# Optimization experiments

Measured on AMD Instinct MI355X. Metric: run time of the kernel, lower is better.

The kernel has to match this reference:

```python
import jax, jax.numpy as jnp
import numpy as np

B, T, N = 16, 1024, 128
WIN, STEP = 30, 2
MOMENT_ORDERS = (2, 4, 8)
D_MODEL = 256


def _mask_diag(corr):
    n = corr.shape[-1]
    eye = jnp.eye(n, dtype=corr.dtype)
    return corr * (1.0 - eye) + eye


def corrcoef_time(xw):
    # xw: [..., L, N] -> corr over channels: [..., N, N]
    L = xw.shape[-2]
    xm = xw - xw.mean(axis=-2, keepdims=True)
    cov = jnp.einsum('...ln,...lm->...nm', xm, xm) / (L - 1 + 1e-8)
    var = jnp.clip(jnp.diagonal(cov, axis1=-2, axis2=-1), 1e-8, None)
    std = jnp.sqrt(var)
    corr = cov / (std[..., :, None] * std[..., None, :])
    corr = jnp.nan_to_num(corr, nan=0.0, posinf=0.0, neginf=0.0)
    return _mask_diag(corr)


def rowwise_corr(M):
    # M: [B, N, F]
    Xc = M - M.mean(axis=-1, keepdims=True)
    num = jnp.einsum('bnf,bmf->bnm', Xc, Xc)
    den1 = jnp.sqrt(jnp.clip((Xc ** 2).sum(axis=-1), 1e-8, None))
    corr = num / (den1[:, :, None] * den1[:, None, :])
    corr = jnp.nan_to_num(corr, nan=0.0, posinf=0.0, neginf=0.0)
    return _mask_diag(corr)


def layer_norm(x, gamma, beta, eps=1e-5):
    mu = x.mean(axis=-1, keepdims=True)
    var = ((x - mu) ** 2).mean(axis=-1, keepdims=True)
    return (x - mu) / jnp.sqrt(var + eps) * gamma + beta


def normalize_adj(adj):
    n = adj.shape[-1]
    A_hat = adj + jnp.eye(n, dtype=adj.dtype)
    d = A_hat.sum(axis=-1)
    dis = jnp.sqrt(1.0 / jnp.clip(d, 1e-8, None))
    return A_hat * dis[:, :, None] * dis[:, None, :]


def setup_inputs() -> dict:
    key = jax.random.key(0)
    ks = jax.random.split(key, 8)
    in_dim = len(MOMENT_ORDERS) * N
    return {
        'x': jax.random.normal(ks[0], (B, T, N), dtype=jnp.float32),
        'ln_gamma': jnp.ones((in_dim,), jnp.float32),
        'ln_beta': jnp.zeros((in_dim,), jnp.float32),
        'W1': jax.random.normal(ks[1], (in_dim, D_MODEL), jnp.float32) * 0.05,
        'b1': jnp.zeros((D_MODEL,), jnp.float32),
        'W2': jax.random.normal(ks[2], (D_MODEL, D_MODEL), jnp.float32) * 0.05,
        'b2': jnp.zeros((D_MODEL,), jnp.float32),
        'Wc': jax.random.normal(ks[3], (D_MODEL, 1), jnp.float32) * 0.05,
        'bc': jnp.zeros((1,), jnp.float32),
    }


def reference(x, ln_gamma, ln_beta, W1, b1, W2, b2, Wc, bc):
    # sliding windows (static indices)
    starts = np.arange(0, T - WIN + 1, STEP)
    idx = starts[:, None] + np.arange(WIN)[None, :]
    xw = x[:, idx, :]
    lo = corrcoef_time(xw)                            # [B, Wn, N, N]

    mean_lo = lo.mean(axis=1, keepdims=True)
    centered = lo - mean_lo
    cm_list, ho_list = [], []
    for d in MOMENT_ORDERS:
        cm = jnp.nan_to_num((centered ** d).mean(axis=1),
                            nan=0.0, posinf=0.0, neginf=0.0)  # [B, N, N]
        cm_list.append(cm)
        ho_list.append(rowwise_corr(cm))

    X = jnp.concatenate(cm_list, axis=-1)             # [B, N, 3N]
    X = layer_norm(X, ln_gamma, ln_beta)

    A = jnp.stack(ho_list, axis=1).mean(axis=1)
    A = 0.5 * (A + jnp.swapaxes(A, 1, 2))
    A_norm = normalize_adj(A)

    H = jax.nn.relu(jnp.einsum('bnm,bmd->bnd', A_norm, X @ W1 + b1))
    H = jax.nn.relu(jnp.einsum('bnm,bmd->bnd', A_norm, H @ W2 + b2))
    g = H.mean(axis=1)                                # [B, d_model]
    out = jax.nn.sigmoid(g @ Wc + bc)                 # [B, 1]
    return out
```

## Files before the change

### kernel.cpp

```cpp
#include <hip/hip_runtime.h>
#include <math.h>

#define BB  16
#define TT  1024
#define NN  128
#define WIN 30
#define NWD 498
#define DM  256
#define IND 384
#define GW  8

#define INV_W (1.0f/498.0f)

#define SARR (BB*NN*NN)

#define OFF_A     0
#define OFF_G     (OFF_A    + BB*NWD*NN)
#define OFF_CM2   (OFF_G    + BB*NWD*NN)
#define OFF_CM4   (OFF_CM2  + SARR)
#define OFF_CM8   (OFF_CM4  + SARR)
#define OFF_AD    (OFF_CM8  + SARR)
#define OFF_PART  (OFF_AD   + 3*SARR)
#define OFF_ANORM OFF_PART
#define OFF_BUFA  (OFF_ANORM + SARR)
#define OFF_BUFB  (OFF_BUFA + BB*NN*DM)
#define OFF_CTR   (OFF_PART + 768*16384)
#define OFF_GW1   OFF_A
#define OFF_SG    (OFF_GW1 + IND*DM)
#define OFF_SB    (OFF_SG  + DM)

#define GLL16(gsrc, ldst) \
    __builtin_amdgcn_global_load_lds((const __attribute__((address_space(1))) void*)(gsrc), \
                                     (__attribute__((address_space(3))) void*)(ldst), 16, 0, 0)

__global__ __launch_bounds__(128) void k1_stats(const float* __restrict__ x, float* __restrict__ ws) {
    int bx = blockIdx.x;
    if (bx == 0 && threadIdx.x < 128) ((unsigned*)(ws + OFF_CTR))[threadIdx.x] = 0u;
    int c = bx & 15, b = bx >> 4;
    int w0 = c*32, w1 = min(NWD, w0+32);
    int n = threadIdx.x;
    const float* xp = x + (size_t)b*TT*NN + n;

    float sum = 0.f, sq = 0.f;
    for (int t = 2*w0; t < 2*w0 + WIN; ++t) {
        float v = xp[(size_t)t*NN];
        sum += v; sq = fmaf(v, v, sq);
    }
    for (int w = w0; w < w1; ++w) {
        if (w > w0) {
            float o0 = xp[(size_t)(2*w-2)*NN], o1 = xp[(size_t)(2*w-1)*NN];
            float n0 = xp[(size_t)(2*w+28)*NN], n1 = xp[(size_t)(2*w+29)*NN];
            sum += (n0 + n1) - (o0 + o1);
            sq  += (n0*n0 + n1*n1) - (o0*o0 + o1*o1);
        }
        float mean = sum * (1.0f/30.0f);
        float ss = sq - 30.0f*mean*mean;
        float var = fmaxf(ss * (1.0f/29.0f), 1e-8f);
        float a = (1.0f / sqrtf(var)) * 0.185695338f;
        ws[OFF_A + ((size_t)b*NWD + w)*NN + n] = a;
        ws[OFF_G + ((size_t)b*NWD + w)*NN + n] = mean * a * 5.477225575f;
    }
}

__global__ __launch_bounds__(256) __attribute__((amdgpu_waves_per_eu(4, 4)))
void k24_inc(const float* __restrict__ x, float* __restrict__ ws) {
    __shared__ __align__(16) float xr[64][NN];
    __shared__ __align__(16) float sa[GW][NN];
    __shared__ __align__(16) float sg[GW][NN];
    int bx = blockIdx.x;
    int wc = bx & 7;
    int slab = (bx >> 3) % 6;
    int b = bx / 48;
    const char IS[6] = {0,0,0,0,1,1};
    const char JS[6] = {0,1,2,3,2,3};
    int is = IS[slab], js = JS[slab];
    int w0 = wc * 63, w1 = min(NWD, w0 + 63);
    int tid = threadIdx.x;
    int jg = tid & 7, ig = tid >> 3;
    int i0 = is*64 + ig*2;
    int j0 = js*32 + jg*4;

    const float* xb = x + (size_t)b*TT*NN;
    const float* Ab = ws + OFF_A + (size_t)b*NWD*NN;
    const float* Gb = ws + OFF_G + (size_t)b*NWD*NN;

    float P[2][4];
    float S1[2][4], S2[2][4], S3[2][4], S4[2][4], S5[2][4], S6[2][4], S7[2][4], S8[2][4];
#pragma unroll
    for (int p=0;p<2;++p)
#pragma unroll
        for (int q=0;q<4;++q) {
            P[p][q]=0.f;
            S1[p][q]=0.f;S2[p][q]=0.f;S3[p][q]=0.f;S4[p][q]=0.f;
            S5[p][q]=0.f;S6[p][q]=0.f;S7[p][q]=0.f;S8[p][q]=0.f;
        }

    auto moments = [&](int k) {
        float2 ai = *(const float2*)&sa[k][i0];
        float2 gi = *(const float2*)&sg[k][i0];
        float4 aj = *(const float4*)&sa[k][j0];
        float4 gj = *(const float4*)&sg[k][j0];
        float av[2] = {ai.x, ai.y};
        float mg[2] = {-gi.x, -gi.y};
        float aw[4] = {aj.x, aj.y, aj.z, aj.w};
        float gw[4] = {gj.x, gj.y, gj.z, gj.w};
#pragma unroll
        for (int p=0;p<2;++p)
#pragma unroll
            for (int q=0;q<4;++q) {
                float aa  = av[p]*aw[q];
                float ngg = mg[p]*gw[q];
                float c   = fmaf(P[p][q], aa, ngg);
                float c2 = c*c;
                float c3 = c2*c;
                float c4 = c2*c2;
                S1[p][q] += c;
                S2[p][q] += c2;
                S3[p][q] += c3;
                S4[p][q] += c4;
                S5[p][q] = fmaf(c4, c,  S5[p][q]);
                S6[p][q] = fmaf(c3, c3, S6[p][q]);
                S7[p][q] = fmaf(c3, c4, S7[p][q]);
                S8[p][q] = fmaf(c4, c4, S8[p][q]);
            }
    };

    int rlo = 2*w0;
    for (int wg = w0; wg < w1; wg += GW) {
        int m = min(GW, w1 - wg);
        __syncthreads();
        int rhi = 2*(wg + m - 1) + 29;
        int nr = rhi - rlo + 1;
        for (int idx = tid; idx < nr*32; idx += 256) {
            int r = idx >> 5, c4 = idx & 31;
            int t = rlo + r;
            GLL16(xb + (size_t)t*NN + c4*4, &xr[t & 63][c4*4]);
        }
        for (int idx = tid; idx < m*32; idx += 256) {
            int k = idx >> 5, c4 = idx & 31;
            GLL16(Ab + (size_t)(wg+k)*NN + c4*4, &sa[k][c4*4]);
        }
        for (int idx = tid; idx < m*32; idx += 256) {
            int k = idx >> 5, c4 = idx & 31;
            GLL16(Gb + (size_t)(wg+k)*NN + c4*4, &sg[k][c4*4]);
        }
        rlo = rhi + 1;
        __syncthreads();

        int kstart = 0;
        if (wg == w0) {
#pragma unroll 6
            for (int k = 0; k < WIN; ++k) {
                int t = 2*w0 + k;
                float2 xi = *(const float2*)&xr[t & 63][i0];
                float4 xj = *(const float4*)&xr[t & 63][j0];
                float av[2] = {xi.x, xi.y};
                float bv[4] = {xj.x, xj.y, xj.z, xj.w};
#pragma unroll
                for (int p=0;p<2;++p)
#pragma unroll
                    for (int q=0;q<4;++q) P[p][q] = fmaf(av[p], bv[q], P[p][q]);
            }
            moments(0);
            kstart = 1;
        }
        for (int k = kstart; k < m; ++k) {
            int w = wg + k;
            int tr[4] = {2*w - 2, 2*w - 1, 2*w + 28, 2*w + 29};
#pragma unroll
            for (int kk = 0; kk < 4; ++kk) {
                int t = tr[kk];
                float sgn = (kk < 2) ? -1.0f : 1.0f;
                float2 xi = *(const float2*)&xr[t & 63][i0];
                float4 xj = *(const float4*)&xr[t & 63][j0];
                float av[2] = {sgn*xi.x, sgn*xi.y};
                float bv[4] = {xj.x, xj.y, xj.z, xj.w};
#pragma unroll
                for (int p=0;p<2;++p)
#pragma unroll
                    for (int q=0;q<4;++q) P[p][q] = fmaf(av[p], bv[q], P[p][q]);
            }
            moments(k);
        }
    }

    float* tp = ws + OFF_PART + (size_t)bx*16384 + tid*8;
#define STORE_ARR(A, S) \
    *(float4*)&tp[(A)*2048]     = make_float4(S[0][0], S[0][1], S[0][2], S[0][3]); \
    *(float4*)&tp[(A)*2048 + 4] = make_float4(S[1][0], S[1][1], S[1][2], S[1][3]);
    STORE_ARR(0, S1) STORE_ARR(1, S2) STORE_ARR(2, S3) STORE_ARR(3, S4)
    STORE_ARR(4, S5) STORE_ARR(5, S6) STORE_ARR(6, S7) STORE_ARR(7, S8)
#undef STORE_ARR
}

__global__ __launch_bounds__(256) void kred(const float* __restrict__ gamma, const float* __restrict__ beta,
                                            const float* __restrict__ W1, float* __restrict__ ws) {
    int bxg = blockIdx.x;
    int tid = threadIdx.x;
    if (bxg >= 192) {
        int gi = bxg - 192;
        if (gi < 96) {
#pragma unroll
            for (int kk = 0; kk < 4; ++kk) {
                int k = gi*4 + kk;
                ws[OFF_GW1 + (size_t)k*DM + tid] = gamma[k] * W1[(size_t)k*DM + tid];
            }
        } else {
            float sgv = 0.f, sbv = 0.f;
            for (int k = 0; k < IND; ++k) {
                float w = W1[(size_t)k*DM + tid];
                sgv = fmaf(gamma[k], w, sgv);
                sbv = fmaf(beta[k],  w, sbv);
            }
            ws[OFF_SG + tid] = sgv;
            ws[OFF_SB + tid] = sbv;
        }
        return;
    }
    int pair = bxg >> 1, half = bxg & 1;
    int b = pair / 6, slab = pair % 6;
    const char IS[6] = {0,0,0,0,1,1};
    const char JS[6] = {0,1,2,3,2,3};
    int is = IS[slab], js = JS[slab];
    int off4 = half*256 + tid;
    const float4* base = (const float4*)(ws + OFF_PART + (size_t)(b*48 + slab*8)*16384);

    float4 E[8];
#pragma unroll
    for (int a=0;a<8;++a) E[a] = make_float4(0.f,0.f,0.f,0.f);
    for (int c = 0; c < 8; ++c) {
        const float4* tp = base + (size_t)c*4096;
#pragma unroll
        for (int a=0;a<8;++a) {
            float4 v = tp[a*512 + off4];
            E[a].x += v.x; E[a].y += v.y; E[a].z += v.z; E[a].w += v.w;
        }
    }
    float Es[8][4];
#pragma unroll
    for (int a=0;a<8;++a) { Es[a][0]=E[a].x; Es[a][1]=E[a].y; Es[a][2]=E[a].z; Es[a][3]=E[a].w; }

    int tid_old = off4 >> 1, p = off4 & 1;
    int ig = tid_old >> 3, jg = tid_old & 7;
    int i  = is*64 + ig*2 + p;
    int j0 = js*32 + jg*4;
    float* C2 = ws + OFF_CM2 + (size_t)b*NN*NN;
    float* C4 = ws + OFF_CM4 + (size_t)b*NN*NN;
    float* C8 = ws + OFF_CM8 + (size_t)b*NN*NN;
#pragma unroll
    for (int l = 0; l < 4; ++l) {
        int j = j0 + l;
        float cm2, cm4, cm8;
        if (i == j) {
            cm2 = 0.f; cm4 = 0.f; cm8 = 0.f;
        } else {
            float e1 = Es[0][l]*INV_W, e2 = Es[1][l]*INV_W, e3 = Es[2][l]*INV_W, e4 = Es[3][l]*INV_W;
            float e5 = Es[4][l]*INV_W, e6 = Es[5][l]*INV_W, e7 = Es[6][l]*INV_W, e8 = Es[7][l]*INV_W;
            float m  = e1;
            float m2 = m*m, m3 = m2*m, m4 = m2*m2, m5 = m4*m, m6 = m3*m3, m8 = m4*m4;
            cm2 = e2 - m2;
            cm4 = e4 - 4.f*m*e3 + 6.f*m2*e2 - 3.f*m4;
            cm8 = e8 - 8.f*m*e7 + 28.f*m2*e6 - 56.f*m3*e5 + 70.f*m4*e4
                     - 56.f*m5*e3 + 28.f*m6*e2 - 7.f*m8;
        }
        C2[i*NN + j] = cm2; C2[j*NN + i] = cm2;
        C4[i*NN + j] = cm4; C4[j*NN + i] = cm4;
        C8[i*NN + j] = cm8; C8[j*NN + i] = cm8;
    }
}

#define XSTR 132
__global__ __launch_bounds__(256) void kB(const float* __restrict__ b1, float* __restrict__ ws) {
    __shared__ __align__(16) float smem[64*XSTR + 2*NN];
    __shared__ unsigned winB;
    int blk = blockIdx.x, tid = threadIdx.x;
    if (blk < 192) {
        int rem = blk % 12;
        int b = blk / 12, di = rem >> 2, jq = rem & 3;
        float* Xct = smem;
        float* Mr  = smem + 64*XSTR;
        float* Ir  = Mr + NN;
        const float* cm = ws + (di==0 ? OFF_CM2 : (di==1 ? OFF_CM4 : OFF_CM8)) + (size_t)b*NN*NN;
        int n0 = (tid >> 4)*8, m0 = jq*32 + (tid & 15)*2;
        float s1 = 0.f, s2 = 0.f;
        float acc0[8], acc1[8];
#pragma unroll
        for (int k=0;k<8;++k) { acc0[k]=0.f; acc1[k]=0.f; }

        for (int h = 0; h < 2; ++h) {
            __syncthreads();
            for (int idx = tid; idx < NN*64; idx += 256) {
                int n = idx >> 6, f0 = idx & 63;
                Xct[f0*XSTR + n] = cm[n*NN + h*64 + f0];
            }
            __syncthreads();
            if (tid < NN) {
                for (int f0 = 0; f0 < 64; ++f0) {
                    float v = Xct[f0*XSTR + tid];
                    s1 += v; s2 = fmaf(v, v, s2);
                }
            }
            for (int f0 = 0; f0 < 64; ++f0) {
                const float* row = &Xct[f0*XSTR];
                float4 a0 = *(const float4*)&row[n0];
                float4 a1 = *(const float4*)&row[n0+4];
                float2 bm = *(const float2*)&row[m0];
                float av[8] = {a0.x,a0.y,a0.z,a0.w,a1.x,a1.y,a1.z,a1.w};
#pragma unroll
                for (int k=0;k<8;++k) {
                    acc0[k] = fmaf(av[k], bm.x, acc0[k]);
                    acc1[k] = fmaf(av[k], bm.y, acc1[k]);
                }
            }
        }
        __syncthreads();
        if (tid < NN) {
            float mean = s1 * (1.0f/NN);
            Mr[tid] = mean;
            Ir[tid] = 1.0f/sqrtf(fmaxf(s2 - (float)NN*mean*mean, 1e-8f));
        }
        __syncthreads();
        float rm0 = Mr[m0], rm1 = Mr[m0+1], im0 = Ir[m0], im1 = Ir[m0+1];
        float* Ad = ws + OFF_AD + (size_t)(b*3 + di)*NN*NN;
#pragma unroll
        for (int k=0;k<8;++k) {
            int gi = n0+k;
            float rn = Mr[gi], inv = Ir[gi];
            float v0 = (acc0[k] - (float)NN*rn*rm0) * inv * im0;
            float v1 = (acc1[k] - (float)NN*rn*rm1) * inv * im1;
            if (gi == m0)   v0 = 1.0f;
            if (gi == m0+1) v1 = 1.0f;
            Ad[gi*NN + m0]     = v0;
            Ad[gi*NN + m0 + 1] = v1;
        }

        __syncthreads();
        if (tid == 0) {
            unsigned* ctr = (unsigned*)(ws + OFF_CTR);
            unsigned old = __hip_atomic_fetch_add(&ctr[96 + b], 1u,
                                                  __ATOMIC_ACQ_REL, __HIP_MEMORY_SCOPE_AGENT);
            winB = (old == 11u) ? 1u : 0u;
        }
        __syncthreads();
        if (winB) {
            float* dis = smem;
            const float* A0 = ws + OFF_AD + (size_t)(b*3 + 0)*NN*NN;
            const float* A1 = ws + OFF_AD + (size_t)(b*3 + 1)*NN*NN;
            const float* A2 = ws + OFF_AD + (size_t)(b*3 + 2)*NN*NN;
            if (tid < NN) {
                float d = 1.0f;
                for (int m = 0; m < NN; ++m) {
                    int o = tid*NN + m;
                    d += (A0[o] + A1[o] + A2[o]) * (1.0f/3.0f);
                }
                dis[tid] = sqrtf(1.0f / fmaxf(d, 1e-8f));
            }
            __syncthreads();
            float* An = ws + OFF_ANORM + (size_t)b*NN*NN;
            for (int idx = tid; idx < NN*NN; idx += 256) {
                int n = idx >> 7, m = idx & 127;
                float s = (A0[idx] + A1[idx] + A2[idx]) * (1.0f/3.0f);
                float v = s + (n==m ? 1.0f : 0.0f);
                An[idx] = v * dis[n] * dis[m];
            }
        }
    } else {
        int r0 = (blk - 192) * 4;
        float* sms = smem;
        float* srs = smem + 4;
        {
            int rloc = tid >> 6, lane = tid & 63;
            int grow = r0 + rloc;
            int b = grow >> 7, n = grow & 127;
            const float* c2 = ws + OFF_CM2 + ((size_t)b*NN + n)*NN;
            const float* c4 = ws + OFF_CM4 + ((size_t)b*NN + n)*NN;
            const float* c8 = ws + OFF_CM8 + ((size_t)b*NN + n)*NN;
            float s1 = 0.f, s2 = 0.f;
            for (int e = lane; e < IND; e += 64) {
                float v = (e < 128) ? c2[e] : (e < 256) ? c4[e-128] : c8[e-256];
                s1 += v; s2 = fmaf(v, v, s2);
            }
#pragma unroll
            for (int o = 32; o > 0; o >>= 1) {
                s1 += __shfl_down(s1, o, 64);
                s2 += __shfl_down(s2, o, 64);
            }
            if (lane == 0) {
                float mean = s1 * (1.0f/IND);
                sms[rloc] = mean;
                srs[rloc] = 1.0f / sqrtf(s2*(1.0f/IND) - mean*mean + 1e-5f);
            }
        }
        __syncthreads();
        float mean[4], rstd[4];
        const float* xrow[4];
#pragma unroll
        for (int r = 0; r < 4; ++r) {
            mean[r] = sms[r]; rstd[r] = srs[r];
        }
        float acc[4] = {0.f, 0.f, 0.f, 0.f};
        const float* GW1p = ws + OFF_GW1;
#pragma unroll
        for (int seg = 0; seg < 3; ++seg) {
            int offc = (seg==0) ? OFF_CM2 : (seg==1) ? OFF_CM4 : OFF_CM8;
#pragma unroll
            for (int r = 0; r < 4; ++r) {
                int grow = r0 + r;
                xrow[r] = ws + offc + ((size_t)(grow >> 7)*NN + (grow & 127))*NN;
            }
            const float* gseg = GW1p + (size_t)(seg*128)*DM + tid;
            for (int k = 0; k < 128; k += 2) {
                float g0 = gseg[(size_t)(k+0)*DM];
                float g1 = gseg[(size_t)(k+1)*DM];
#pragma unroll
                for (int r = 0; r < 4; ++r) {
                    acc[r] = fmaf(xrow[r][k+0], g0, acc[r]);
                    acc[r] = fmaf(xrow[r][k+1], g1, acc[r]);
                }
            }
        }
        float sgv = ws[OFF_SG + tid];
        float sbb = ws[OFF_SB + tid] + b1[tid];
        float* O = ws + OFF_BUFA;
#pragma unroll
        for (int r = 0; r < 4; ++r)
            O[(size_t)(r0+r)*DM + tid] = rstd[r]*(acc[r] - mean[r]*sgv) + sbb;
    }
}

__global__ __launch_bounds__(256) void k98_propgemm(const float* __restrict__ W2, const float* __restrict__ b2,
                                                    const float* __restrict__ An, const float* __restrict__ Zin,
                                                    float* __restrict__ Out) {
    __shared__ float Hs[4][DM];
    int bx = blockIdx.x;
    int b = bx >> 5, n0 = (bx & 31)*4;
    int tid = threadIdx.x;
    const float* A = An + (size_t)b*NN*NN + (size_t)n0*NN;
    const float* Z = Zin + (size_t)b*NN*DM;
    float acc[4] = {0,0,0,0};
    for (int m = 0; m < NN; m += 4) {
        float z0 = Z[(size_t)(m+0)*DM + tid];
        float z1 = Z[(size_t)(m+1)*DM + tid];
        float z2 = Z[(size_t)(m+2)*DM + tid];
        float z3 = Z[(size_t)(m+3)*DM + tid];
#pragma unroll
        for (int r = 0; r < 4; ++r) {
            const float* Ar = A + r*NN + m;
            acc[r] = fmaf(Ar[0], z0, acc[r]);
            acc[r] = fmaf(Ar[1], z1, acc[r]);
            acc[r] = fmaf(Ar[2], z2, acc[r]);
            acc[r] = fmaf(Ar[3], z3, acc[r]);
        }
    }
#pragma unroll
    for (int r = 0; r < 4; ++r) Hs[r][tid] = fmaxf(acc[r], 0.0f);
    __syncthreads();
    float acc2[4];
    float bv = b2[tid];
#pragma unroll
    for (int r = 0; r < 4; ++r) acc2[r] = bv;
    for (int k = 0; k < DM; k += 4) {
        float w0 = W2[(size_t)(k+0)*DM + tid];
        float w1 = W2[(size_t)(k+1)*DM + tid];
        float w2 = W2[(size_t)(k+2)*DM + tid];
        float w3 = W2[(size_t)(k+3)*DM + tid];
#pragma unroll
        for (int r = 0; r < 4; ++r) {
            float4 h = *(const float4*)&Hs[r][k];
            acc2[r] = fmaf(h.x, w0, acc2[r]);
            acc2[r] = fmaf(h.y, w1, acc2[r]);
            acc2[r] = fmaf(h.z, w2, acc2[r]);
            acc2[r] = fmaf(h.w, w3, acc2[r]);
        }
    }
    float* O = Out + (size_t)b*NN*DM;
#pragma unroll
    for (int r = 0; r < 4; ++r) O[(size_t)(n0+r)*DM + tid] = acc2[r];
}

__global__ __launch_bounds__(256) void k9_prop(const float* __restrict__ Wc, const float* __restrict__ bc,
                                               const float* __restrict__ An, const float* __restrict__ Zin,
                                               float* __restrict__ Out,
                                               float* __restrict__ ws, float* __restrict__ outp) {
    __shared__ float red[256];
    __shared__ unsigned win9;
    int bx = blockIdx.x;
    int b = bx >> 5, n0 = (bx & 31)*4;
    int tid = threadIdx.x;
    const float* A = An + (size_t)b*NN*NN + (size_t)n0*NN;
    const float* Z = Zin + (size_t)b*NN*DM;
    float acc[4] = {0,0,0,0};
    for (int m = 0; m < NN; m += 4) {
        float z0 = Z[(size_t)(m+0)*DM + tid];
        float z1 = Z[(size_t)(m+1)*DM + tid];
        float z2 = Z[(size_t)(m+2)*DM + tid];
        float z3 = Z[(size_t)(m+3)*DM + tid];
#pragma unroll
        for (int r = 0; r < 4; ++r) {
            const float* Ar = A + r*NN + m;
            acc[r] = fmaf(Ar[0], z0, acc[r]);
            acc[r] = fmaf(Ar[1], z1, acc[r]);
            acc[r] = fmaf(Ar[2], z2, acc[r]);
            acc[r] = fmaf(Ar[3], z3, acc[r]);
        }
    }
    float* O = Out + (size_t)b*NN*DM;
#pragma unroll
    for (int r = 0; r < 4; ++r) O[(size_t)(n0+r)*DM + tid] = fmaxf(acc[r], 0.0f);

    __syncthreads();
    if (tid == 0) {
        unsigned* ctr = (unsigned*)(ws + OFF_CTR);
        unsigned old = __hip_atomic_fetch_add(&ctr[112 + b], 1u,
                                              __ATOMIC_ACQ_REL, __HIP_MEMORY_SCOPE_AGENT);
        win9 = (old == 31u) ? 1u : 0u;
    }
    __syncthreads();
    if (win9) {
        const float* H = Out + (size_t)b*NN*DM;
        float s = 0.f;
        for (int n = 0; n < NN; ++n) s += H[(size_t)n*DM + tid];
        red[tid] = s * (1.0f/NN) * Wc[tid];
        __syncthreads();
        for (int o = 128; o > 0; o >>= 1) { if (tid < o) red[tid] += red[tid+o]; __syncthreads(); }
        if (tid == 0) outp[b] = 1.0f/(1.0f + expf(-(red[0] + bc[0])));
    }
}

extern "C" void kernel_launch(void* const* d_in, const int* in_sizes, int n_in,
                              void* d_out, int out_size, void* d_ws, size_t ws_size,
                              hipStream_t stream) {
    (void)in_sizes; (void)n_in; (void)out_size; (void)ws_size;
    const float* x     = (const float*)d_in[0];
    const float* gamma = (const float*)d_in[1];
    const float* beta  = (const float*)d_in[2];
    const float* W1    = (const float*)d_in[3];
    const float* b1    = (const float*)d_in[4];
    const float* W2    = (const float*)d_in[5];
    const float* b2    = (const float*)d_in[6];
    const float* Wc    = (const float*)d_in[7];
    const float* bc    = (const float*)d_in[8];
    float* ws  = (float*)d_ws;
    float* out = (float*)d_out;

    k1_stats    <<<BB*16,    128, 0, stream>>>(x, ws);
    k24_inc     <<<BB*6*8,   256, 0, stream>>>(x, ws);
    kred        <<<192+96+1, 256, 0, stream>>>(gamma, beta, W1, ws);
    kB          <<<704,      256, 0, stream>>>(b1, ws);
    k98_propgemm<<<BB*32,    256, 0, stream>>>(W2, b2, ws + OFF_ANORM, ws + OFF_BUFA, ws + OFF_BUFB);
    k9_prop     <<<BB*32,    256, 0, stream>>>(Wc, bc, ws + OFF_ANORM, ws + OFF_BUFB, ws + OFF_BUFA, ws, out);
}
```

Baseline: 238.5 us.

## Replace last-block atomic counters with atomic row sums and separate tail kernels

The last-block-wins pattern in kB (adjacency normalization) and k9_prop (graph pooling head) is removed. kB now accumulates adjacency row sums with warp shuffles and float atomics, and a new small kernel builds the normalized adjacency. k9_prop reduces its rows straight into per-batch atomic sums, so the H buffer is no longer written, and a one-block head kernel applies the sigmoid. GW in k24_inc is doubled and its waves-per-EU target lowered. This removes serialized tail work on one block per batch, at the cost of two extra launches and order-dependent float atomics.

```diff
diff --git a/kernel.cpp b/kernel.cpp
--- a/kernel.cpp
+++ b/kernel.cpp
@@ -8,7 +8,7 @@
 #define NWD 498
 #define DM  256
 #define IND 384
-#define GW  8
+#define GW  16
 
 #define INV_W (1.0f/498.0f)
 
@@ -24,7 +24,7 @@
 #define OFF_ANORM OFF_PART
 #define OFF_BUFA  (OFF_ANORM + SARR)
 #define OFF_BUFB  (OFF_BUFA + BB*NN*DM)
-#define OFF_CTR   (OFF_PART + 768*16384)
+#define OFF_AUX   (OFF_PART + 768*16384)
 #define OFF_GW1   OFF_A
 #define OFF_SG    (OFF_GW1 + IND*DM)
 #define OFF_SB    (OFF_SG  + DM)
@@ -35,7 +35,9 @@
 
 __global__ __launch_bounds__(128) void k1_stats(const float* __restrict__ x, float* __restrict__ ws) {
     int bx = blockIdx.x;
-    if (bx == 0 && threadIdx.x < 128) ((unsigned*)(ws + OFF_CTR))[threadIdx.x] = 0u;
+    if (bx == 0) {
+        for (int i = threadIdx.x; i < 2064; i += 128) ws[OFF_AUX + i] = 0.f;
+    }
     int c = bx & 15, b = bx >> 4;
     int w0 = c*32, w1 = min(NWD, w0+32);
     int n = threadIdx.x;
@@ -62,7 +64,7 @@
     }
 }
 
-__global__ __launch_bounds__(256) __attribute__((amdgpu_waves_per_eu(4, 4)))
+__global__ __launch_bounds__(256) __attribute__((amdgpu_waves_per_eu(3, 3)))
 void k24_inc(const float* __restrict__ x, float* __restrict__ ws) {
     __shared__ __align__(16) float xr[64][NN];
     __shared__ __align__(16) float sa[GW][NN];
@@ -272,7 +274,6 @@
 #define XSTR 132
 __global__ __launch_bounds__(256) void kB(const float* __restrict__ b1, float* __restrict__ ws) {
     __shared__ __align__(16) float smem[64*XSTR + 2*NN];
-    __shared__ unsigned winB;
     int blk = blockIdx.x, tid = threadIdx.x;
     if (blk < 192) {
         int rem = blk % 12;
@@ -322,6 +323,8 @@
         __syncthreads();
         float rm0 = Mr[m0], rm1 = Mr[m0+1], im0 = Ir[m0], im1 = Ir[m0+1];
         float* Ad = ws + OFF_AD + (size_t)(b*3 + di)*NN*NN;
+        float* rowsum = ws + OFF_AUX + (size_t)b*NN;
+        int l = tid & 15;
 #pragma unroll
         for (int k=0;k<8;++k) {
             int gi = n0+k;
@@ -332,37 +335,10 @@
             if (gi == m0+1) v1 = 1.0f;
             Ad[gi*NN + m0]     = v0;
             Ad[gi*NN + m0 + 1] = v1;
-        }
-
-        __syncthreads();
-        if (tid == 0) {
-            unsigned* ctr = (unsigned*)(ws + OFF_CTR);
-            unsigned old = __hip_atomic_fetch_add(&ctr[96 + b], 1u,
-                                                  __ATOMIC_ACQ_REL, __HIP_MEMORY_SCOPE_AGENT);
-            winB = (old == 11u) ? 1u : 0u;
-        }
-        __syncthreads();
-        if (winB) {
-            float* dis = smem;
-            const float* A0 = ws + OFF_AD + (size_t)(b*3 + 0)*NN*NN;
-            const float* A1 = ws + OFF_AD + (size_t)(b*3 + 1)*NN*NN;
-            const float* A2 = ws + OFF_AD + (size_t)(b*3 + 2)*NN*NN;
-            if (tid < NN) {
-                float d = 1.0f;
-                for (int m = 0; m < NN; ++m) {
-                    int o = tid*NN + m;
-                    d += (A0[o] + A1[o] + A2[o]) * (1.0f/3.0f);
-                }
-                dis[tid] = sqrtf(1.0f / fmaxf(d, 1e-8f));
-            }
-            __syncthreads();
-            float* An = ws + OFF_ANORM + (size_t)b*NN*NN;
-            for (int idx = tid; idx < NN*NN; idx += 256) {
-                int n = idx >> 7, m = idx & 127;
-                float s = (A0[idx] + A1[idx] + A2[idx]) * (1.0f/3.0f);
-                float v = s + (n==m ? 1.0f : 0.0f);
-                An[idx] = v * dis[n] * dis[m];
-            }
+            float s = v0 + v1;
+#pragma unroll
+            for (int o = 8; o > 0; o >>= 1) s += __shfl_down(s, o, 16);
+            if (l == 0) atomicAdd(&rowsum[gi], s * (1.0f/3.0f));
         }
     } else {
         int r0 = (blk - 192) * 4;
@@ -428,6 +404,27 @@
     }
 }
 
+__global__ __launch_bounds__(256) void k6_anorm(float* __restrict__ ws) {
+    __shared__ float dis[NN];
+    int b = blockIdx.x, tid = threadIdx.x;
+    const float* rowsum = ws + OFF_AUX + (size_t)b*NN;
+    if (tid < NN) {
+        float d = 1.0f + rowsum[tid];
+        dis[tid] = sqrtf(1.0f / fmaxf(d, 1e-8f));
+    }
+    __syncthreads();
+    const float* A0 = ws + OFF_AD + (size_t)(b*3 + 0)*NN*NN;
+    const float* A1 = ws + OFF_AD + (size_t)(b*3 + 1)*NN*NN;
+    const float* A2 = ws + OFF_AD + (size_t)(b*3 + 2)*NN*NN;
+    float* An = ws + OFF_ANORM + (size_t)b*NN*NN;
+    for (int idx = tid; idx < NN*NN; idx += 256) {
+        int n = idx >> 7, m = idx & 127;
+        float s = (A0[idx] + A1[idx] + A2[idx]) * (1.0f/3.0f);
+        float v = s + (n==m ? 1.0f : 0.0f);
+        An[idx] = v * dis[n] * dis[m];
+    }
+}
+
 __global__ __launch_bounds__(256) void k98_propgemm(const float* __restrict__ W2, const float* __restrict__ b2,
                                                     const float* __restrict__ An, const float* __restrict__ Zin,
                                                     float* __restrict__ Out) {
@@ -478,12 +475,10 @@
     for (int r = 0; r < 4; ++r) O[(size_t)(n0+r)*DM + tid] = acc2[r];
 }
 
-__global__ __launch_bounds__(256) void k9_prop(const float* __restrict__ Wc, const float* __restrict__ bc,
+__global__ __launch_bounds__(256) void k9_prop(const float* __restrict__ Wc,
                                                const float* __restrict__ An, const float* __restrict__ Zin,
-                                               float* __restrict__ Out,
-                                               float* __restrict__ ws, float* __restrict__ outp) {
+                                               float* __restrict__ ws) {
     __shared__ float red[256];
-    __shared__ unsigned win9;
     int bx = blockIdx.x;
     int b = bx >> 5, n0 = (bx & 31)*4;
     int tid = threadIdx.x;
@@ -504,26 +499,20 @@
             acc[r] = fmaf(Ar[3], z3, acc[r]);
         }
     }
-    float* O = Out + (size_t)b*NN*DM;
-#pragma unroll
-    for (int r = 0; r < 4; ++r) O[(size_t)(n0+r)*DM + tid] = fmaxf(acc[r], 0.0f);
-
+    float hsum = fmaxf(acc[0], 0.0f) + fmaxf(acc[1], 0.0f)
+               + fmaxf(acc[2], 0.0f) + fmaxf(acc[3], 0.0f);
+    red[tid] = hsum * Wc[tid];
     __syncthreads();
-    if (tid == 0) {
-        unsigned* ctr = (unsigned*)(ws + OFF_CTR);
-        unsigned old = __hip_atomic_fetch_add(&ctr[112 + b], 1u,
-                                              __ATOMIC_ACQ_REL, __HIP_MEMORY_SCOPE_AGENT);
-        win9 = (old == 31u) ? 1u : 0u;
-    }
-    __syncthreads();
-    if (win9) {
-        const float* H = Out + (size_t)b*NN*DM;
-        float s = 0.f;
-        for (int n = 0; n < NN; ++n) s += H[(size_t)n*DM + tid];
-        red[tid] = s * (1.0f/NN) * Wc[tid];
-        __syncthreads();
-        for (int o = 128; o > 0; o >>= 1) { if (tid < o) red[tid] += red[tid+o]; __syncthreads(); }
-        if (tid == 0) outp[b] = 1.0f/(1.0f + expf(-(red[0] + bc[0])));
+    for (int o = 128; o > 0; o >>= 1) { if (tid < o) red[tid] += red[tid+o]; __syncthreads(); }
+    if (tid == 0) atomicAdd(ws + OFF_AUX + 2048 + b, red[0]);
+}
+
+__global__ __launch_bounds__(64) void k12_head(const float* __restrict__ bc,
+                                               const float* __restrict__ ws, float* __restrict__ outp) {
+    int tid = threadIdx.x;
+    if (tid < BB) {
+        float g = ws[OFF_AUX + 2048 + tid] * (1.0f/NN);
+        outp[tid] = 1.0f/(1.0f + expf(-(g + bc[0])));
     }
 }
 
@@ -547,6 +536,8 @@
     k24_inc     <<<BB*6*8,   256, 0, stream>>>(x, ws);
     kred        <<<192+96+1, 256, 0, stream>>>(gamma, beta, W1, ws);
     kB          <<<704,      256, 0, stream>>>(b1, ws);
+    k6_anorm    <<<BB,       256, 0, stream>>>(ws);
     k98_propgemm<<<BB*32,    256, 0, stream>>>(W2, b2, ws + OFF_ANORM, ws + OFF_BUFA, ws + OFF_BUFB);
-    k9_prop     <<<BB*32,    256, 0, stream>>>(Wc, bc, ws + OFF_ANORM, ws + OFF_BUFB, ws + OFF_BUFA, ws, out);
-}
+    k9_prop     <<<BB*32,    256, 0, stream>>>(Wc, ws + OFF_ANORM, ws + OFF_BUFB, ws);
+    k12_head    <<<1,        64,  0, stream>>>(bc, ws, out);
+}
```

Result: faster. 223.7 us, median of 2 (-6.2%).
